# Performance work log

Hardware: AMD Instinct MI355X
Metric: run time of the kernel (lower is better)

The kernel has to match this reference:

```python
import jax, jax.numpy as jnp
import numpy as np

H, N, M = 1024, 128, 512
EPS_COS = 1e-8


def setup_inputs() -> dict:
    key = jax.random.key(0)
    ks = iter(jax.random.split(key, 64))
    def rn(shape, s=0.02):
        return jax.random.normal(next(ks), shape, jnp.float32) * s
    x = jax.random.normal(next(ks), (1, H), jnp.float32)
    prw = jax.random.uniform(next(ks), (1, N), jnp.float32)
    prev_read_w = prw / jnp.sum(prw, axis=1, keepdims=True)
    pww = jax.random.uniform(next(ks), (1, N), jnp.float32)
    prev_write_w = pww / jnp.sum(pww, axis=1, keepdims=True)
    inp = {
        "x": x,
        "prev_read_w": prev_read_w,
        "prev_write_w": prev_write_w,
        "h0": rn((1, H), 0.1),
        "c0": rn((1, H), 0.1),
        "memory": jnp.ones((N, M), jnp.float32),
        "W_ih": rn((4 * H, H)), "W_hh": rn((4 * H, H)),
        "b_ih": rn((4 * H,)), "b_hh": rn((4 * H,)),
        "rk_w": rn((M, H)), "rk_b": rn((M,)),
        "rbeta_w": rn((1, H)), "rbeta_b": rn((1,)),
        "rg_w": rn((1, H)), "rg_b": rn((1,)),
        "rs_w": rn((N, H)), "rs_b": rn((N,)),
        "rgamma_w": rn((1, H)), "rgamma_b": rn((1,)),
        "wk_w": rn((M, H)), "wk_b": rn((M,)),
        "wbeta_w": rn((1, H)), "wbeta_b": rn((1,)),
        "wg_w": rn((1, H)), "wg_b": rn((1,)),
        "ws_w": rn((N, H)), "ws_b": rn((N,)),
        "wgamma_w": rn((1, H)), "wgamma_b": rn((1,)),
        "we_w": rn((N * M, H)), "we_b": rn((N * M,)),
        "wa_w": rn((M, H)), "wa_b": rn((M,)),
        "fc_w": rn((H, H + M)), "fc_b": rn((H,)),
    }
    return inp


def _lstm_cell(x, h, c, W_ih, W_hh, b_ih, b_hh):
    # torch gate order: i, f, g, o
    gates = x @ W_ih.T + b_ih + h @ W_hh.T + b_hh  # (1, 4H)
    i, f, g, o = jnp.split(gates, 4, axis=1)
    c_new = jax.nn.sigmoid(f) * c + jax.nn.sigmoid(i) * jnp.tanh(g)
    h_new = jax.nn.sigmoid(o) * jnp.tanh(c_new)
    return h_new, c_new


def _address(x, prev_w, mem, k_w, k_b, beta_w, beta_b, g_w, g_b, s_w, s_b, gamma_w, gamma_b):
    k = x @ k_w.T + k_b                                  # (1, M)
    beta = jax.nn.softplus(x @ beta_w.T + beta_b)        # (1, 1)
    g = jax.nn.sigmoid(x @ g_w.T + g_b)                  # (1, 1)
    s = jax.nn.softmax(x @ s_w.T + s_b, axis=-1)         # (1, N)
    gamma = 1.0 + jax.nn.softplus(x @ gamma_w.T + gamma_b)  # (1, 1)
    # cosine similarity of each memory row with k
    mem_n = jnp.maximum(jnp.linalg.norm(mem, axis=1), EPS_COS)     # (N,)
    k_n = jnp.maximum(jnp.linalg.norm(k[0]), EPS_COS)
    cos = (mem @ k[0]) / (mem_n * k_n)                   # (N,)
    w_c = jax.nn.softmax(beta * cos[None, :], axis=1)    # (1, N)
    w_g = g * w_c + (1.0 - g) * prev_w                   # (1, N)
    # circular convolution: w_t[i] = sum_j w_g[j] * s[(i - j) mod N]
    idx = (jnp.arange(N)[:, None] - jnp.arange(N)[None, :]) % N    # (N, N)
    w_t = (s[0][idx] @ w_g[0])[None, :]                  # (1, N)
    w = w_t ** gamma
    w = w / (jnp.sum(w, axis=1, keepdims=True) + 1e-16)
    return w


def reference(x, prev_read_w, prev_write_w, h0, c0, memory,
              W_ih, W_hh, b_ih, b_hh,
              rk_w, rk_b, rbeta_w, rbeta_b, rg_w, rg_b, rs_w, rs_b, rgamma_w, rgamma_b,
              wk_w, wk_b, wbeta_w, wbeta_b, wg_w, wg_b, ws_w, ws_b, wgamma_w, wgamma_b,
              we_w, we_b, wa_w, wa_b, fc_w, fc_b):
    sg = jax.lax.stop_gradient
    # controller (single LSTM step, batch 1)
    h, c = _lstm_cell(x, h0, c0, W_ih, W_hh, b_ih, b_hh)
    co = h  # controller output (1, H)
    mem = sg(memory)  # memory is detached in the original
    # read head
    rw = _address(co, prev_read_w, mem, rk_w, rk_b, rbeta_w, rbeta_b,
                  rg_w, rg_b, rs_w, rs_b, rgamma_w, rgamma_b)
    read = rw @ mem                                      # (1, M)
    # write head (note: receives prev_read_w, faithful to source)
    ww = _address(co, prev_read_w, mem, wk_w, wk_b, wbeta_w, wbeta_b,
                  wg_w, wg_b, ws_w, ws_b, wgamma_w, wgamma_b)
    e = jax.nn.sigmoid(co @ we_w.T + we_b)               # (1, N*M)
    a = co @ wa_w.T + wa_b                               # (1, M)
    # memory write with detached w, e, a (as in original)
    ww_d, e_d, a_d = sg(ww), sg(e), sg(a)
    new_mem = memory * (1.0 - ww_d @ e_d.reshape(N, M))  # (1,M) broadcast over (N,M)
    new_mem = new_mem + ww_d.T * a_d                     # (N,1)*(1,M)
    # output projection
    fc_in = jnp.concatenate([co, read], axis=1)          # (1, H+M)
    out = fc_in @ fc_w.T + fc_b                          # (1, H)
    return (out, sg(rw), sg(ww), h, c, new_mem)
```

## Files before the change

### kernel.cpp

```cpp
#include <hip/hip_runtime.h>
#include <math.h>

#define HH 1024
#define NN 128
#define MM 512

#define OFF_RW 1024
#define OFF_WW 1152
#define OFF_H  1280
#define OFF_C  2304
#define OFF_NM 3328

#define WS_GATES   0
#define WS_CO      4096
#define WS_MNORM   5120
#define WS_A       5248
#define WS_KR      5760
#define WS_KW      6272
#define WS_RSLOG   6784
#define WS_WSLOG   6912
#define WS_FCPART  7040
#define WS_SCAL    8064
#define WS_WWV     8072
#define WS_ERASE   8200
#define WS_READ    8712

__device__ __forceinline__ float sigmoidf_(float z) { return 1.f / (1.f + expf(-z)); }
__device__ __forceinline__ float softplusf_(float z) {
    return fmaxf(z, 0.f) + log1pf(expf(-fabsf(z)));
}
__device__ __forceinline__ float wave_reduce(float v) {
    #pragma unroll
    for (int off = 32; off > 0; off >>= 1) v += __shfl_down(v, off, 64);
    return v;
}

__global__ __launch_bounds__(256) void k1_gates_norms(
    const float* __restrict__ x, const float* __restrict__ h0,
    const float* __restrict__ W_ih, const float* __restrict__ W_hh,
    const float* __restrict__ b_ih, const float* __restrict__ b_hh,
    const float* __restrict__ memory, float* __restrict__ gates,
    float* __restrict__ mem_norm)
{
    int t = threadIdx.x, lane = t & 63, wv = t >> 6;
    if (blockIdx.x < 1024) {
        int r = blockIdx.x * 4 + wv;
        const float4* wi = (const float4*)(W_ih + (long long)r * HH);
        const float4* wh = (const float4*)(W_hh + (long long)r * HH);
        const float4* x4 = (const float4*)x;
        const float4* h4 = (const float4*)h0;
        float acc = 0.f;
        #pragma unroll
        for (int q = 0; q < 4; ++q) {
            float4 aa = wi[q * 64 + lane], bb = x4[q * 64 + lane];
            acc += aa.x * bb.x + aa.y * bb.y + aa.z * bb.z + aa.w * bb.w;
        }
        #pragma unroll
        for (int q = 0; q < 4; ++q) {
            float4 aa = wh[q * 64 + lane], bb = h4[q * 64 + lane];
            acc += aa.x * bb.x + aa.y * bb.y + aa.z * bb.z + aa.w * bb.w;
        }
        acc = wave_reduce(acc);
        if (lane == 0) gates[r] = acc + b_ih[r] + b_hh[r];
    } else {
        int n = (blockIdx.x - 1024) * 4 + wv;
        const float4* r4 = (const float4*)(memory + n * MM);
        float acc = 0.f;
        #pragma unroll
        for (int q = 0; q < 2; ++q) {
            float4 aa = r4[q * 64 + lane];
            acc += aa.x * aa.x + aa.y * aa.y + aa.z * aa.z + aa.w * aa.w;
        }
        acc = wave_reduce(acc);
        if (lane == 0) mem_norm[n] = sqrtf(acc);
    }
}

__global__ __launch_bounds__(256) void k2_lstm(
    const float* __restrict__ gates, const float* __restrict__ c0,
    float* __restrict__ out, float* __restrict__ co, float* __restrict__ erase)
{
    int j = blockIdx.x * 256 + threadIdx.x;
    float gi = gates[j], gf = gates[j + 1024], gg = gates[j + 2048], go = gates[j + 3072];
    float cn = sigmoidf_(gf) * c0[j] + sigmoidf_(gi) * tanhf(gg);
    float hn = sigmoidf_(go) * tanhf(cn);
    out[OFF_H + j] = hn;
    out[OFF_C + j] = cn;
    co[j] = hn;
    if (j < 512) erase[j] = 0.f;
}

#define K3S_ROWS 2822
__global__ __launch_bounds__(256) void k3_small(
    const float* __restrict__ co,
    const float* __restrict__ wa_w, const float* __restrict__ wa_b,
    const float* __restrict__ rk_w, const float* __restrict__ rk_b,
    const float* __restrict__ wk_w, const float* __restrict__ wk_b,
    const float* __restrict__ rs_w, const float* __restrict__ rs_b,
    const float* __restrict__ sw_w, const float* __restrict__ sw_b,
    const float* __restrict__ fc_w, const float* __restrict__ fc_b,
    const float* __restrict__ rbeta_w, const float* __restrict__ rbeta_b,
    const float* __restrict__ rg_w, const float* __restrict__ rg_b,
    const float* __restrict__ rgamma_w, const float* __restrict__ rgamma_b,
    const float* __restrict__ wbeta_w, const float* __restrict__ wbeta_b,
    const float* __restrict__ wg_w, const float* __restrict__ wg_b,
    const float* __restrict__ wgamma_w, const float* __restrict__ wgamma_b,
    float* __restrict__ a, float* __restrict__ kr, float* __restrict__ kw,
    float* __restrict__ rs_logit, float* __restrict__ ws_logit,
    float* __restrict__ fc_part, float* __restrict__ scal)
{
    int t = threadIdx.x, lane = t & 63, wv = t >> 6;
    int r = blockIdx.x * 4 + wv;
    if (r >= K3S_ROWS) return;
    const float* row;
    float bias = 0.f;
    float* dst;
    if (r < 512) {
        row = wa_w + (long long)r * HH; if (lane == 0) bias = wa_b[r]; dst = a + r;
    } else if (r < 1024) {
        int i = r - 512; row = rk_w + (long long)i * HH; if (lane == 0) bias = rk_b[i]; dst = kr + i;
    } else if (r < 1536) {
        int i = r - 1024; row = wk_w + (long long)i * HH; if (lane == 0) bias = wk_b[i]; dst = kw + i;
    } else if (r < 1664) {
        int i = r - 1536; row = rs_w + (long long)i * HH; if (lane == 0) bias = rs_b[i]; dst = rs_logit + i;
    } else if (r < 1792) {
        int i = r - 1664; row = sw_w + (long long)i * HH; if (lane == 0) bias = sw_b[i]; dst = ws_logit + i;
    } else if (r < 2816) {
        int i = r - 1792; row = fc_w + (long long)i * 1536; if (lane == 0) bias = fc_b[i]; dst = fc_part + i;
    } else {
        int i = r - 2816;
        const float* wsrc; const float* bsrc;
        switch (i) {
            case 0: wsrc = rbeta_w;  bsrc = rbeta_b;  break;
            case 1: wsrc = rg_w;     bsrc = rg_b;     break;
            case 2: wsrc = rgamma_w; bsrc = rgamma_b; break;
            case 3: wsrc = wbeta_w;  bsrc = wbeta_b;  break;
            case 4: wsrc = wg_w;     bsrc = wg_b;     break;
            default: wsrc = wgamma_w; bsrc = wgamma_b; break;
        }
        row = wsrc; if (lane == 0) bias = bsrc[0]; dst = scal + i;
    }
    const float4* r4 = (const float4*)row;
    const float4* c4 = (const float4*)co;
    float acc = 0.f;
    #pragma unroll
    for (int q = 0; q < 4; ++q) {
        float4 aa = r4[q * 64 + lane], bb = c4[q * 64 + lane];
        acc += aa.x * bb.x + aa.y * bb.y + aa.z * bb.z + aa.w * bb.w;
    }
    acc = wave_reduce(acc);
    if (lane == 0) *dst = acc + bias;
}

__global__ __launch_bounds__(256) void k4_address(
    const float* __restrict__ kr, const float* __restrict__ kw,
    const float* __restrict__ scal,
    const float* __restrict__ rs_logit, const float* __restrict__ ws_logit,
    const float* __restrict__ prev_w, const float* __restrict__ mem_norm,
    const float* __restrict__ memory,
    float* __restrict__ out, float* __restrict__ wwv, float* __restrict__ readv)
{
    int head = blockIdx.x;
    int t = threadIdx.x, lane = t & 63, wv = t >> 6;
    const float* k = head ? kw : kr;
    const float* slog = head ? ws_logit : rs_logit;
    float beta  = softplusf_(scal[head ? 3 : 0]);
    float gg    = sigmoidf_(scal[head ? 4 : 1]);
    float gamma = 1.f + softplusf_(scal[head ? 5 : 2]);

    __shared__ float tmp[256];
    __shared__ float s_cos[128];
    __shared__ float s_s[128];
    __shared__ float s_wg[128];
    __shared__ float s_w[128];

    float a0 = k[t], a1 = k[t + 256];
    tmp[t] = a0 * a0 + a1 * a1;
    __syncthreads();
    for (int off = 128; off > 0; off >>= 1) { if (t < off) tmp[t] += tmp[t + off]; __syncthreads(); }
    float k_norm = sqrtf(tmp[0]);
    __syncthreads();

    for (int i = 0; i < 32; ++i) {
        int n = wv * 32 + i;
        const float4* r4 = (const float4*)(memory + n * MM);
        const float4* k4 = (const float4*)k;
        float acc = 0.f;
        #pragma unroll
        for (int q = 0; q < 2; ++q) {
            float4 aa = r4[q * 64 + lane], bb = k4[q * 64 + lane];
            acc += aa.x * bb.x + aa.y * bb.y + aa.z * bb.z + aa.w * bb.w;
        }
        acc = wave_reduce(acc);
        if (lane == 0)
            s_cos[n] = acc / (fmaxf(mem_norm[n], 1e-8f) * fmaxf(k_norm, 1e-8f));
    }
    __syncthreads();

    float z = (t < 128) ? beta * s_cos[t] : -1e30f;
    tmp[t] = z; __syncthreads();
    for (int off = 128; off > 0; off >>= 1) { if (t < off) tmp[t] = fmaxf(tmp[t], tmp[t + off]); __syncthreads(); }
    float zmax = tmp[0]; __syncthreads();
    float ez = (t < 128) ? expf(z - zmax) : 0.f;
    tmp[t] = ez; __syncthreads();
    for (int off = 128; off > 0; off >>= 1) { if (t < off) tmp[t] += tmp[t + off]; __syncthreads(); }
    float zsum = tmp[0]; __syncthreads();
    if (t < 128) s_wg[t] = gg * (ez / zsum) + (1.f - gg) * prev_w[t];

    float sl = (t < 128) ? slog[t] : -1e30f;
    tmp[t] = sl; __syncthreads();
    for (int off = 128; off > 0; off >>= 1) { if (t < off) tmp[t] = fmaxf(tmp[t], tmp[t + off]); __syncthreads(); }
    float smax = tmp[0]; __syncthreads();
    float es = (t < 128) ? expf(sl - smax) : 0.f;
    tmp[t] = es; __syncthreads();
    for (int off = 128; off > 0; off >>= 1) { if (t < off) tmp[t] += tmp[t + off]; __syncthreads(); }
    float ssum = tmp[0]; __syncthreads();
    if (t < 128) s_s[t] = es / ssum;
    __syncthreads();

    float wt = 0.f;
    if (t < 128) {
        #pragma unroll 8
        for (int j = 0; j < 128; ++j) wt += s_wg[j] * s_s[(t - j) & 127];
        wt = powf(wt, gamma);
    }
    tmp[t] = (t < 128) ? wt : 0.f;
    __syncthreads();
    for (int off = 128; off > 0; off >>= 1) { if (t < off) tmp[t] += tmp[t + off]; __syncthreads(); }
    float wsum = tmp[0]; __syncthreads();
    if (t < 128) {
        float wf = wt / (wsum + 1e-16f);
        out[(head ? OFF_WW : OFF_RW) + t] = wf;
        s_w[t] = wf;
        if (head) wwv[t] = wf;
    }
    __syncthreads();

    if (head == 0) {
        for (int m = t; m < MM; m += 256) {
            float acc = 0.f;
            #pragma unroll 4
            for (int n = 0; n < NN; ++n) acc += s_w[n] * memory[n * MM + m];
            readv[m] = acc;
        }
    }
}

__global__ __launch_bounds__(256) void k5_bige(
    const float* __restrict__ co,
    const float* __restrict__ we_w, const float* __restrict__ we_b,
    const float* __restrict__ wwv, float* __restrict__ erase)
{
    int t = threadIdx.x, lane = t & 63, wv = t >> 6;
    int wid = blockIdx.x * 4 + wv;
    long long r0 = (long long)wid * 2;
    const float4* w0 = (const float4*)(we_w + r0 * HH);
    const float4* w1 = (const float4*)(we_w + (r0 + 1) * HH);
    const float4* c4 = (const float4*)co;
    float acc0 = 0.f, acc1 = 0.f;
    #pragma unroll
    for (int q = 0; q < 4; ++q) {
        float4 bb = c4[q * 64 + lane];
        float4 a0 = w0[q * 64 + lane];
        float4 a1 = w1[q * 64 + lane];
        acc0 += a0.x * bb.x + a0.y * bb.y + a0.z * bb.z + a0.w * bb.w;
        acc1 += a1.x * bb.x + a1.y * bb.y + a1.z * bb.z + a1.w * bb.w;
    }
    acc0 = wave_reduce(acc0);
    acc1 = wave_reduce(acc1);
    if (lane == 0) {
        int n0 = (int)(r0 >> 9), m0 = (int)(r0 & 511);
        float e0 = sigmoidf_(acc0 + we_b[r0]);
        float e1 = sigmoidf_(acc1 + we_b[r0 + 1]);
        atomicAdd(&erase[m0], wwv[n0] * e0);
        int n1 = (int)((r0 + 1) >> 9), m1 = (int)((r0 + 1) & 511);
        atomicAdd(&erase[m1], wwv[n1] * e1);
    }
}

__global__ __launch_bounds__(256) void k6_final(
    const float* __restrict__ memory, const float* __restrict__ erase,
    const float* __restrict__ wwv, const float* __restrict__ a,
    const float* __restrict__ fc_w, const float* __restrict__ fc_part,
    const float* __restrict__ readv, float* __restrict__ out)
{
    int b = blockIdx.x, t = threadIdx.x;
    if (b < 256) {
        int idx = b * 256 + t;
        int n = idx >> 9, m = idx & 511;
        out[OFF_NM + idx] = memory[idx] * (1.f - erase[m]) + wwv[n] * a[m];
    } else {
        int w = (b - 256) * 4 + (t >> 6);
        int lane = t & 63;
        const float4* r4 = (const float4*)(fc_w + (long long)w * 1536 + 1024);
        const float4* v4 = (const float4*)readv;
        float acc = 0.f;
        #pragma unroll
        for (int q = 0; q < 2; ++q) {
            float4 aa = r4[q * 64 + lane], bb = v4[q * 64 + lane];
            acc += aa.x * bb.x + aa.y * bb.y + aa.z * bb.z + aa.w * bb.w;
        }
        acc = wave_reduce(acc);
        if (lane == 0) out[w] = fc_part[w] + acc;
    }
}

extern "C" void kernel_launch(void* const* d_in, const int* in_sizes, int n_in,
                              void* d_out, int out_size, void* d_ws, size_t ws_size,
                              hipStream_t stream)
{
    const float* x           = (const float*)d_in[0];
    const float* prev_read_w = (const float*)d_in[1];
    const float* h0      = (const float*)d_in[3];
    const float* c0      = (const float*)d_in[4];
    const float* memory  = (const float*)d_in[5];
    const float* W_ih    = (const float*)d_in[6];
    const float* W_hh    = (const float*)d_in[7];
    const float* b_ih    = (const float*)d_in[8];
    const float* b_hh    = (const float*)d_in[9];
    const float* rk_w    = (const float*)d_in[10];
    const float* rk_b    = (const float*)d_in[11];
    const float* rbeta_w = (const float*)d_in[12];
    const float* rbeta_b = (const float*)d_in[13];
    const float* rg_w    = (const float*)d_in[14];
    const float* rg_b    = (const float*)d_in[15];
    const float* rs_w    = (const float*)d_in[16];
    const float* rs_b    = (const float*)d_in[17];
    const float* rgamma_w = (const float*)d_in[18];
    const float* rgamma_b = (const float*)d_in[19];
    const float* wk_w    = (const float*)d_in[20];
    const float* wk_b    = (const float*)d_in[21];
    const float* wbeta_w = (const float*)d_in[22];
    const float* wbeta_b = (const float*)d_in[23];
    const float* wg_w    = (const float*)d_in[24];
    const float* wg_b    = (const float*)d_in[25];
    const float* sw_w    = (const float*)d_in[26];
    const float* sw_b    = (const float*)d_in[27];
    const float* wgamma_w = (const float*)d_in[28];
    const float* wgamma_b = (const float*)d_in[29];
    const float* we_w    = (const float*)d_in[30];
    const float* we_b    = (const float*)d_in[31];
    const float* wa_w    = (const float*)d_in[32];
    const float* wa_b    = (const float*)d_in[33];
    const float* fc_w    = (const float*)d_in[34];
    const float* fc_b    = (const float*)d_in[35];

    float* ws  = (float*)d_ws;
    float* out = (float*)d_out;

    float* gates    = ws + WS_GATES;
    float* co       = ws + WS_CO;
    float* mem_norm = ws + WS_MNORM;
    float* a        = ws + WS_A;
    float* kr       = ws + WS_KR;
    float* kw       = ws + WS_KW;
    float* rs_logit = ws + WS_RSLOG;
    float* ws_logit = ws + WS_WSLOG;
    float* fc_part  = ws + WS_FCPART;
    float* scal     = ws + WS_SCAL;
    float* wwv      = ws + WS_WWV;
    float* erase    = ws + WS_ERASE;
    float* readv    = ws + WS_READ;

    k1_gates_norms<<<1056, 256, 0, stream>>>(x, h0, W_ih, W_hh, b_ih, b_hh,
                                             memory, gates, mem_norm);
    k2_lstm<<<4, 256, 0, stream>>>(gates, c0, out, co, erase);
    k3_small<<<(K3S_ROWS + 3) / 4, 256, 0, stream>>>(
        co, wa_w, wa_b, rk_w, rk_b, wk_w, wk_b, rs_w, rs_b, sw_w, sw_b,
        fc_w, fc_b,
        rbeta_w, rbeta_b, rg_w, rg_b, rgamma_w, rgamma_b,
        wbeta_w, wbeta_b, wg_w, wg_b, wgamma_w, wgamma_b,
        a, kr, kw, rs_logit, ws_logit, fc_part, scal);
    k4_address<<<2, 256, 0, stream>>>(kr, kw, scal, rs_logit, ws_logit,
                                      prev_read_w, mem_norm, memory,
                                      out, wwv, readv);
    k5_bige<<<8192, 256, 0, stream>>>(co, we_w, we_b, wwv, erase);
    k6_final<<<512, 256, 0, stream>>>(memory, erase, wwv, a, fc_w, fc_part,
                                      readv, out);
}
```

Measured before the change: 496.4 us.

## Widen address kernel, move read-vector into big erase kernel, use nontemporal loads

The address kernel now runs with 1024 threads per head and uses wave-shuffle block reductions in place of shared-memory tree reductions. The serial read-vector product moves out of the two-block address kernel into two extra blocks of the erase kernel. The erase GEMV now gives each wave four rows and loads weights with nontemporal loads, and the LSTM weight loads are also nontemporal. The aim is to cut the latency of the tiny serial stage and improve streaming bandwidth on the large we_w matrix, at the cost of more atomics per lane and changes to the workspace layout.

New measurement: 469.3 us. 5.4% less time.

```diff
diff --git a/kernel.cpp b/kernel.cpp
--- a/kernel.cpp
+++ b/kernel.cpp
@@ -4,6 +4,8 @@
 #define HH 1024
 #define NN 128
 #define MM 512
+
+typedef float vf4 __attribute__((ext_vector_type(4)));
 
 #define OFF_RW 1024
 #define OFF_WW 1152
@@ -22,8 +24,9 @@
 #define WS_FCPART  7040
 #define WS_SCAL    8064
 #define WS_WWV     8072
-#define WS_ERASE   8200
-#define WS_READ    8712
+#define WS_RWV     8200
+#define WS_ERASE   8328
+#define WS_READ    8840
 
 __device__ __forceinline__ float sigmoidf_(float z) { return 1.f / (1.f + expf(-z)); }
 __device__ __forceinline__ float softplusf_(float z) {
@@ -33,6 +36,31 @@
     #pragma unroll
     for (int off = 32; off > 0; off >>= 1) v += __shfl_down(v, off, 64);
     return v;
+}
+__device__ __forceinline__ float wave_reduce_max(float v) {
+    #pragma unroll
+    for (int off = 32; off > 0; off >>= 1) v = fmaxf(v, __shfl_down(v, off, 64));
+    return v;
+}
+__device__ __forceinline__ float block_sum(float v, float* wred, int t) {
+    __syncthreads();
+    float r = wave_reduce(v);
+    if ((t & 63) == 0) wred[t >> 6] = r;
+    __syncthreads();
+    float s = 0.f;
+    #pragma unroll
+    for (int i = 0; i < 16; ++i) s += wred[i];
+    return s;
+}
+__device__ __forceinline__ float block_max(float v, float* wred, int t) {
+    __syncthreads();
+    float r = wave_reduce_max(v);
+    if ((t & 63) == 0) wred[t >> 6] = r;
+    __syncthreads();
+    float s = -1e30f;
+    #pragma unroll
+    for (int i = 0; i < 16; ++i) s = fmaxf(s, wred[i]);
+    return s;
 }
 
 __global__ __launch_bounds__(256) void k1_gates_norms(
@@ -45,31 +73,33 @@
     int t = threadIdx.x, lane = t & 63, wv = t >> 6;
     if (blockIdx.x < 1024) {
         int r = blockIdx.x * 4 + wv;
-        const float4* wi = (const float4*)(W_ih + (long long)r * HH);
-        const float4* wh = (const float4*)(W_hh + (long long)r * HH);
-        const float4* x4 = (const float4*)x;
-        const float4* h4 = (const float4*)h0;
+        const vf4* wi = (const vf4*)(W_ih + (long long)r * HH);
+        const vf4* wh = (const vf4*)(W_hh + (long long)r * HH);
+        const vf4* x4 = (const vf4*)x;
+        const vf4* h4 = (const vf4*)h0;
         float acc = 0.f;
         #pragma unroll
         for (int q = 0; q < 4; ++q) {
-            float4 aa = wi[q * 64 + lane], bb = x4[q * 64 + lane];
-            acc += aa.x * bb.x + aa.y * bb.y + aa.z * bb.z + aa.w * bb.w;
+            vf4 aa = __builtin_nontemporal_load(&wi[q * 64 + lane]);
+            vf4 bb = x4[q * 64 + lane];
+            acc += aa[0] * bb[0] + aa[1] * bb[1] + aa[2] * bb[2] + aa[3] * bb[3];
         }
         #pragma unroll
         for (int q = 0; q < 4; ++q) {
-            float4 aa = wh[q * 64 + lane], bb = h4[q * 64 + lane];
-            acc += aa.x * bb.x + aa.y * bb.y + aa.z * bb.z + aa.w * bb.w;
+            vf4 aa = __builtin_nontemporal_load(&wh[q * 64 + lane]);
+            vf4 bb = h4[q * 64 + lane];
+            acc += aa[0] * bb[0] + aa[1] * bb[1] + aa[2] * bb[2] + aa[3] * bb[3];
         }
         acc = wave_reduce(acc);
         if (lane == 0) gates[r] = acc + b_ih[r] + b_hh[r];
     } else {
         int n = (blockIdx.x - 1024) * 4 + wv;
-        const float4* r4 = (const float4*)(memory + n * MM);
+        const vf4* r4 = (const vf4*)(memory + n * MM);
         float acc = 0.f;
         #pragma unroll
         for (int q = 0; q < 2; ++q) {
-            float4 aa = r4[q * 64 + lane];
-            acc += aa.x * aa.x + aa.y * aa.y + aa.z * aa.z + aa.w * aa.w;
+            vf4 aa = r4[q * 64 + lane];
+            acc += aa[0] * aa[0] + aa[1] * aa[1] + aa[2] * aa[2] + aa[3] * aa[3];
         }
         acc = wave_reduce(acc);
         if (lane == 0) mem_norm[n] = sqrtf(acc);
@@ -140,25 +170,25 @@
         }
         row = wsrc; if (lane == 0) bias = bsrc[0]; dst = scal + i;
     }
-    const float4* r4 = (const float4*)row;
-    const float4* c4 = (const float4*)co;
+    const vf4* r4 = (const vf4*)row;
+    const vf4* c4 = (const vf4*)co;
     float acc = 0.f;
     #pragma unroll
     for (int q = 0; q < 4; ++q) {
-        float4 aa = r4[q * 64 + lane], bb = c4[q * 64 + lane];
-        acc += aa.x * bb.x + aa.y * bb.y + aa.z * bb.z + aa.w * bb.w;
+        vf4 aa = r4[q * 64 + lane], bb = c4[q * 64 + lane];
+        acc += aa[0] * bb[0] + aa[1] * bb[1] + aa[2] * bb[2] + aa[3] * bb[3];
     }
     acc = wave_reduce(acc);
     if (lane == 0) *dst = acc + bias;
 }
 
-__global__ __launch_bounds__(256) void k4_address(
+__global__ __launch_bounds__(1024) void k4_address(
     const float* __restrict__ kr, const float* __restrict__ kw,
     const float* __restrict__ scal,
     const float* __restrict__ rs_logit, const float* __restrict__ ws_logit,
     const float* __restrict__ prev_w, const float* __restrict__ mem_norm,
     const float* __restrict__ memory,
-    float* __restrict__ out, float* __restrict__ wwv, float* __restrict__ readv)
+    float* __restrict__ out, float* __restrict__ rwv, float* __restrict__ wwv)
 {
     int head = blockIdx.x;
     int t = threadIdx.x, lane = t & 63, wv = t >> 6;
@@ -168,29 +198,23 @@
     float gg    = sigmoidf_(scal[head ? 4 : 1]);
     float gamma = 1.f + softplusf_(scal[head ? 5 : 2]);
 
-    __shared__ float tmp[256];
+    __shared__ float wred[16];
     __shared__ float s_cos[128];
     __shared__ float s_s[128];
     __shared__ float s_wg[128];
-    __shared__ float s_w[128];
-
-    float a0 = k[t], a1 = k[t + 256];
-    tmp[t] = a0 * a0 + a1 * a1;
-    __syncthreads();
-    for (int off = 128; off > 0; off >>= 1) { if (t < off) tmp[t] += tmp[t + off]; __syncthreads(); }
-    float k_norm = sqrtf(tmp[0]);
-    __syncthreads();
-
-    for (int i = 0; i < 32; ++i) {
-        int n = wv * 32 + i;
-        const float4* r4 = (const float4*)(memory + n * MM);
-        const float4* k4 = (const float4*)k;
-        float acc = 0.f;
-        #pragma unroll
-        for (int q = 0; q < 2; ++q) {
-            float4 aa = r4[q * 64 + lane], bb = k4[q * 64 + lane];
-            acc += aa.x * bb.x + aa.y * bb.y + aa.z * bb.z + aa.w * bb.w;
-        }
+
+    float kv = (t < 512) ? k[t] : 0.f;
+    float k_norm = sqrtf(block_sum(kv * kv, wred, t));
+
+    const vf4* k4p = (const vf4*)k;
+    vf4 bb0 = k4p[lane], bb1 = k4p[64 + lane];
+    #pragma unroll
+    for (int i = 0; i < 8; ++i) {
+        int n = wv * 8 + i;
+        const vf4* r4 = (const vf4*)(memory + n * MM);
+        vf4 a0 = r4[lane], a1 = r4[64 + lane];
+        float acc = a0[0] * bb0[0] + a0[1] * bb0[1] + a0[2] * bb0[2] + a0[3] * bb0[3]
+                  + a1[0] * bb1[0] + a1[1] * bb1[1] + a1[2] * bb1[2] + a1[3] * bb1[3];
         acc = wave_reduce(acc);
         if (lane == 0)
             s_cos[n] = acc / (fmaxf(mem_norm[n], 1e-8f) * fmaxf(k_norm, 1e-8f));
@@ -198,23 +222,15 @@
     __syncthreads();
 
     float z = (t < 128) ? beta * s_cos[t] : -1e30f;
-    tmp[t] = z; __syncthreads();
-    for (int off = 128; off > 0; off >>= 1) { if (t < off) tmp[t] = fmaxf(tmp[t], tmp[t + off]); __syncthreads(); }
-    float zmax = tmp[0]; __syncthreads();
+    float zmax = block_max(z, wred, t);
     float ez = (t < 128) ? expf(z - zmax) : 0.f;
-    tmp[t] = ez; __syncthreads();
-    for (int off = 128; off > 0; off >>= 1) { if (t < off) tmp[t] += tmp[t + off]; __syncthreads(); }
-    float zsum = tmp[0]; __syncthreads();
+    float zsum = block_sum(ez, wred, t);
     if (t < 128) s_wg[t] = gg * (ez / zsum) + (1.f - gg) * prev_w[t];
 
     float sl = (t < 128) ? slog[t] : -1e30f;
-    tmp[t] = sl; __syncthreads();
-    for (int off = 128; off > 0; off >>= 1) { if (t < off) tmp[t] = fmaxf(tmp[t], tmp[t + off]); __syncthreads(); }
-    float smax = tmp[0]; __syncthreads();
+    float smax = block_max(sl, wred, t);
     float es = (t < 128) ? expf(sl - smax) : 0.f;
-    tmp[t] = es; __syncthreads();
-    for (int off = 128; off > 0; off >>= 1) { if (t < off) tmp[t] += tmp[t + off]; __syncthreads(); }
-    float ssum = tmp[0]; __syncthreads();
+    float ssum = block_sum(es, wred, t);
     if (t < 128) s_s[t] = es / ssum;
     __syncthreads();
 
@@ -224,57 +240,66 @@
         for (int j = 0; j < 128; ++j) wt += s_wg[j] * s_s[(t - j) & 127];
         wt = powf(wt, gamma);
     }
-    tmp[t] = (t < 128) ? wt : 0.f;
-    __syncthreads();
-    for (int off = 128; off > 0; off >>= 1) { if (t < off) tmp[t] += tmp[t + off]; __syncthreads(); }
-    float wsum = tmp[0]; __syncthreads();
+    float wsum = block_sum((t < 128) ? wt : 0.f, wred, t);
     if (t < 128) {
         float wf = wt / (wsum + 1e-16f);
         out[(head ? OFF_WW : OFF_RW) + t] = wf;
-        s_w[t] = wf;
-        if (head) wwv[t] = wf;
-    }
-    __syncthreads();
-
-    if (head == 0) {
-        for (int m = t; m < MM; m += 256) {
-            float acc = 0.f;
-            #pragma unroll 4
-            for (int n = 0; n < NN; ++n) acc += s_w[n] * memory[n * MM + m];
-            readv[m] = acc;
-        }
+        (head ? wwv : rwv)[t] = wf;
     }
 }
 
 __global__ __launch_bounds__(256) void k5_bige(
     const float* __restrict__ co,
     const float* __restrict__ we_w, const float* __restrict__ we_b,
-    const float* __restrict__ wwv, float* __restrict__ erase)
+    const float* __restrict__ wwv, float* __restrict__ erase,
+    const float* __restrict__ rwv, const float* __restrict__ memory,
+    float* __restrict__ readv)
 {
     int t = threadIdx.x, lane = t & 63, wv = t >> 6;
-    int wid = blockIdx.x * 4 + wv;
-    long long r0 = (long long)wid * 2;
-    const float4* w0 = (const float4*)(we_w + r0 * HH);
-    const float4* w1 = (const float4*)(we_w + (r0 + 1) * HH);
-    const float4* c4 = (const float4*)co;
-    float acc0 = 0.f, acc1 = 0.f;
-    #pragma unroll
-    for (int q = 0; q < 4; ++q) {
-        float4 bb = c4[q * 64 + lane];
-        float4 a0 = w0[q * 64 + lane];
-        float4 a1 = w1[q * 64 + lane];
-        acc0 += a0.x * bb.x + a0.y * bb.y + a0.z * bb.z + a0.w * bb.w;
-        acc1 += a1.x * bb.x + a1.y * bb.y + a1.z * bb.z + a1.w * bb.w;
-    }
-    acc0 = wave_reduce(acc0);
-    acc1 = wave_reduce(acc1);
-    if (lane == 0) {
-        int n0 = (int)(r0 >> 9), m0 = (int)(r0 & 511);
-        float e0 = sigmoidf_(acc0 + we_b[r0]);
-        float e1 = sigmoidf_(acc1 + we_b[r0 + 1]);
-        atomicAdd(&erase[m0], wwv[n0] * e0);
-        int n1 = (int)((r0 + 1) >> 9), m1 = (int)((r0 + 1) & 511);
-        atomicAdd(&erase[m1], wwv[n1] * e1);
+    int b = blockIdx.x;
+    if (b < 4096) {
+        int wid = b * 4 + wv;
+        long long r0 = (long long)wid * 4;
+        const vf4* c4 = (const vf4*)co;
+        const float* base = we_w + r0 * HH;
+        float acc0 = 0.f, acc1 = 0.f, acc2 = 0.f, acc3 = 0.f;
+        #pragma unroll
+        for (int q = 0; q < 4; ++q) {
+            vf4 bb = c4[q * 64 + lane];
+            vf4 a0 = __builtin_nontemporal_load((const vf4*)(base) + q * 64 + lane);
+            vf4 a1 = __builtin_nontemporal_load((const vf4*)(base + HH) + q * 64 + lane);
+            vf4 a2 = __builtin_nontemporal_load((const vf4*)(base + 2 * HH) + q * 64 + lane);
+            vf4 a3 = __builtin_nontemporal_load((const vf4*)(base + 3 * HH) + q * 64 + lane);
+            acc0 += a0[0] * bb[0] + a0[1] * bb[1] + a0[2] * bb[2] + a0[3] * bb[3];
+            acc1 += a1[0] * bb[0] + a1[1] * bb[1] + a1[2] * bb[2] + a1[3] * bb[3];
+            acc2 += a2[0] * bb[0] + a2[1] * bb[1] + a2[2] * bb[2] + a2[3] * bb[3];
+            acc3 += a3[0] * bb[0] + a3[1] * bb[1] + a3[2] * bb[2] + a3[3] * bb[3];
+        }
+        acc0 = wave_reduce(acc0);
+        acc1 = wave_reduce(acc1);
+        acc2 = wave_reduce(acc2);
+        acc3 = wave_reduce(acc3);
+        if (lane == 0) {
+            int n = (int)(r0 >> 9), m0 = (int)(r0 & 511);
+            float wn = wwv[n];
+            float e0 = sigmoidf_(acc0 + we_b[r0]);
+            float e1 = sigmoidf_(acc1 + we_b[r0 + 1]);
+            float e2 = sigmoidf_(acc2 + we_b[r0 + 2]);
+            float e3 = sigmoidf_(acc3 + we_b[r0 + 3]);
+            atomicAdd(&erase[m0],     wn * e0);
+            atomicAdd(&erase[m0 + 1], wn * e1);
+            atomicAdd(&erase[m0 + 2], wn * e2);
+            atomicAdd(&erase[m0 + 3], wn * e3);
+        }
+    } else {
+        __shared__ float s_rw[128];
+        if (t < 128) s_rw[t] = rwv[t];
+        __syncthreads();
+        int m = (b - 4096) * 256 + t;
+        float acc = 0.f;
+        #pragma unroll 4
+        for (int n = 0; n < NN; ++n) acc += s_rw[n] * memory[n * MM + m];
+        readv[m] = acc;
     }
 }
 
@@ -292,13 +317,13 @@
     } else {
         int w = (b - 256) * 4 + (t >> 6);
         int lane = t & 63;
-        const float4* r4 = (const float4*)(fc_w + (long long)w * 1536 + 1024);
-        const float4* v4 = (const float4*)readv;
+        const vf4* r4 = (const vf4*)(fc_w + (long long)w * 1536 + 1024);
+        const vf4* v4 = (const vf4*)readv;
         float acc = 0.f;
         #pragma unroll
         for (int q = 0; q < 2; ++q) {
-            float4 aa = r4[q * 64 + lane], bb = v4[q * 64 + lane];
-            acc += aa.x * bb.x + aa.y * bb.y + aa.z * bb.z + aa.w * bb.w;
+            vf4 aa = r4[q * 64 + lane], bb = v4[q * 64 + lane];
+            acc += aa[0] * bb[0] + aa[1] * bb[1] + aa[2] * bb[2] + aa[3] * bb[3];
         }
         acc = wave_reduce(acc);
         if (lane == 0) out[w] = fc_part[w] + acc;
@@ -359,6 +384,7 @@
     float* fc_part  = ws + WS_FCPART;
     float* scal     = ws + WS_SCAL;
     float* wwv      = ws + WS_WWV;
+    float* rwv      = ws + WS_RWV;
     float* erase    = ws + WS_ERASE;
     float* readv    = ws + WS_READ;
 
@@ -371,10 +397,11 @@
         rbeta_w, rbeta_b, rg_w, rg_b, rgamma_w, rgamma_b,
         wbeta_w, wbeta_b, wg_w, wg_b, wgamma_w, wgamma_b,
         a, kr, kw, rs_logit, ws_logit, fc_part, scal);
-    k4_address<<<2, 256, 0, stream>>>(kr, kw, scal, rs_logit, ws_logit,
-                                      prev_read_w, mem_norm, memory,
-                                      out, wwv, readv);
-    k5_bige<<<8192, 256, 0, stream>>>(co, we_w, we_b, wwv, erase);
+    k4_address<<<2, 1024, 0, stream>>>(kr, kw, scal, rs_logit, ws_logit,
+                                       prev_read_w, mem_norm, memory,
+                                       out, rwv, wwv);
+    k5_bige<<<4098, 256, 0, stream>>>(co, we_w, we_b, wwv, erase,
+                                      rwv, memory, readv);
     k6_final<<<512, 256, 0, stream>>>(memory, erase, wwv, a, fc_w, fc_part,
                                       readv, out);
 }
```
